# Performance work log

Hardware: AMD Instinct MI355X
Metric: run time of the kernel (lower is better)

## Reference

```python
import math
import jax, jax.numpy as jnp
import numpy as np


def _precompute_psi(nlat_in, nlon_in, nlat_out, K, theta_cutoff):
    """Faithful numpy port of _precompute_convolution_tensor (equiangular grids).
    Returns COO indices (k, t, lat_in, lon_in) and float values of the sparse
    filter tensor psi of logical shape [K, nlat_out, nlat_in*nlon_in]."""
    lats_in = np.linspace(0.0, np.pi, nlat_in)
    lats_out = np.linspace(0.0, np.pi, nlat_out)
    phis = np.linspace(-np.pi, np.pi, nlon_in)
    d_theta = theta_cutoff / K
    theta_i = np.arange(K) * d_theta  # (K,)
    ks, ts, las, los, vs = [], [], [], [], []
    alpha = -lats_in[:, None]          # (nlat_in, 1)
    beta = phis[None, :]               # (1, nlon_in)
    for t in range(nlat_out):
        gamma = lats_out[t]
        z = np.cos(alpha) * np.cos(gamma) - np.cos(beta) * np.sin(alpha) * np.sin(gamma)
        theta = np.arccos(np.clip(z, -1.0, 1.0))   # (nlat_in, nlon_in)
        diff = np.abs(theta[None, :, :] - theta_i[:, None, None])  # (K, nlat_in, nlon_in)
        mask = (diff < d_theta) & (theta[None, :, :] < theta_cutoff)
        k_idx, la_idx, lo_idx = np.nonzero(mask)
        v = 1.0 - diff[k_idx, la_idx, lo_idx] / d_theta  # triangle (hat) weights
        ks.append(k_idx); ts.append(np.full_like(k_idx, t)); las.append(la_idx); los.append(lo_idx); vs.append(v)
    return (np.concatenate(ks).astype(np.int32),
            np.concatenate(ts).astype(np.int32),
            np.concatenate(las).astype(np.int32),
            np.concatenate(los).astype(np.int32),
            np.concatenate(vs).astype(np.float32))


def setup_inputs() -> dict:
    B, C = 4, 32
    nlat_in, nlon_in = 361, 720
    nlat_out, nlon_out = 361, 720
    K = 3
    theta_cutoff = 0.01 * math.pi  # default used at the precompute call site
    k, t, la, lo, v = _precompute_psi(nlat_in, nlon_in, nlat_out, K, theta_cutoff)
    key = jax.random.key(0)
    x = jax.random.normal(key, (B, C, nlat_in, nlon_in), dtype=jnp.float32)
    return {
        "x": x,
        "psi_vals": jnp.asarray(v),
        "psi_k": jnp.asarray(k),
        "psi_t": jnp.asarray(t),
        "psi_lat": jnp.asarray(la),
        "psi_lon": jnp.asarray(lo),
        "kernel_size": K,
        "nlat_out": nlat_out,
        "nlon_out": nlon_out,
    }


def reference(x, psi_vals, psi_k, psi_t, psi_lat, psi_lon, kernel_size, nlat_out, nlon_out):
    B, C, nlat_in, nlon_in = x.shape
    BC = B * C
    scale = nlon_in // nlon_out  # = 1 here
    # (nlat_in, nlon_in, BC) layout, matching x.reshape(B*C,...).permute(1,2,0)
    xr = x.reshape(BC, nlat_in, nlon_in).transpose(1, 2, 0)
    seg = psi_k * nlat_out + psi_t           # row id in the (K*nlat_out) output
    num_seg = kernel_size * nlat_out

    def step(_, p):
        # torch.roll(x, scale, dims=lon) applied (p+1) times before the bmm:
        # rolled[lat, lon] = x[lat, (lon - (p+1)*scale) % nlon]
        lon_idx = (psi_lon - (p + 1) * scale) % nlon_in
        g = xr[psi_lat, lon_idx]             # (nnz, BC) irregular gather
        out_p = jax.ops.segment_sum(psi_vals[:, None] * g, seg, num_segments=num_seg)
        return None, out_p                   # (K*nlat_out, BC)

    _, outs = jax.lax.scan(step, None, jnp.arange(nlon_out))  # (nlon_out, K*nlat_out, BC)
    outs = outs.reshape(nlon_out, kernel_size, nlat_out, BC)
    # permute(3,1,2,0) then split BC -> (B, C)
    return outs.transpose(3, 1, 2, 0).reshape(B, C, kernel_size, nlat_out, nlon_out)
```

## Files before the change

kernel.cpp:

```cpp
#include <hip/hip_runtime.h>
#include <math.h>


#define NLAT 361
#define NLON 720
#define KK 3
#define PTILE 48
#define NPX 15
#define NT 384
#define PD 56
#define SWN 832
#define TOTCAP (720*1024)

typedef __attribute__((ext_vector_type(8))) short bf16x8;
typedef __attribute__((ext_vector_type(4))) float f32x4;
typedef __attribute__((ext_vector_type(4))) unsigned int u32x4;

#define D_PI 3.14159265358979311599796346854418516159057617187500
#define STEP_LAT (D_PI / 360.0)
#define STEP_PHI ((2.0 * D_PI) / 719.0)
#define CUTOFF (0.01 * D_PI)
#define DTH (CUTOFF / 3.0)

__device__ __forceinline__ void gll16(const void* g, void* l) {
    __builtin_amdgcn_global_load_lds(
        (const __attribute__((address_space(1))) void*)g,
        (__attribute__((address_space(3))) void*)l, 16, 0, 0);
}

__device__ inline unsigned int bf16pair_rne(float lo, float hi) {
    unsigned int a = __builtin_bit_cast(unsigned int, lo);
    unsigned int b = __builtin_bit_cast(unsigned int, hi);
    a = a + 0x7fffu + ((a >> 16) & 1u);
    b = b + 0x7fffu + ((b >> 16) & 1u);
    return (a >> 16) | (b & 0xffff0000u);
}

__global__ __launch_bounds__(512) void bounds_kernel(int4* __restrict__ params,
                                                     float2* __restrict__ pAB,
                                                     unsigned long long* __restrict__ actd) {
    __shared__ int part[512];
    int tid = threadIdx.x;
    int rmins[9], Ws[9], bl8s[9];
    float As[9], Bs[9];
    int wsum = 0;
    if (tid < NLAT) {
        int t = tid;
        double g = (t == 360) ? D_PI : (double)t * STEP_LAT;
        double cg = cos(g), sg = sin(g);
        const double coscut = cos(CUTOFF);
#pragma unroll
        for (int d = 0; d < 9; ++d) {
            int la = t + d - 4;
            int rmin = 0, W = 0;
            double A = 0.0, Bc = 0.0;
            if (la >= 0 && la <= 360) {
                double lad = (la == 360) ? D_PI : (double)la * STEP_LAT;
                A = cos(lad) * cg;
                Bc = sin(lad) * sg;
                if (Bc < 1e-14) {
                    if (A > coscut) { rmin = 0; W = 720; }
                } else {
                    double C = (coscut - A) / Bc;
                    if (C <= -1.0) { rmin = 0; W = 720; }
                    else if (C < 1.0) {
                        double bmax = acos(C);
                        int r0 = (int)floor((D_PI - bmax) / STEP_PHI) + 1;
                        int r1 = (int)ceil((D_PI + bmax) / STEP_PHI) - 1;
                        if (r0 < 0) r0 = 0;
                        if (r1 > 719) r1 = 719;
                        rmin = r0; W = r1 - r0 + 1;
                        if (W < 0) W = 0;
                    }
                }
            }
            rmins[d] = rmin; Ws[d] = W;
            As[d] = (float)A; Bs[d] = (float)Bc;
            int b8 = 0;
            if (W > 0) {
                b8 = (W + 111) & ~7;
                if (b8 > SWN) b8 = SWN;
            }
            bl8s[d] = b8;
            wsum += b8;
        }
    }
    part[tid] = wsum;
    __syncthreads();
    for (int dd = 1; dd < 512; dd <<= 1) {
        int v = part[tid];
        int w2 = (tid >= dd) ? part[tid - dd] : 0;
        __syncthreads();
        part[tid] = v + w2;
        __syncthreads();
    }
    int base = part[tid] - wsum;
    if (tid < NLAT) {
        unsigned long long pk = 0;
        int nact = 0;
#pragma unroll
        for (int d = 0; d < 9; ++d) {
            int off = base;
            base += bl8s[d];
            if (Ws[d] > 0 && off + bl8s[d] <= TOTCAP) {
                params[tid * 9 + d] = make_int4(rmins[d], Ws[d], off, bl8s[d]);
                pAB[tid * 9 + d] = make_float2(As[d], Bs[d]);
                pk |= ((unsigned long long)d) << (4 + 4 * nact);
                nact++;
            } else {
                params[tid * 9 + d] = make_int4(0, 0, 0, 0);
            }
        }
        pk |= (unsigned long long)nact;
        actd[tid] = pk;
    }
}

__global__ __launch_bounds__(128) void fill_w_kernel(const int4* __restrict__ params,
                                                     const float2* __restrict__ pAB,
                                                     unsigned int* __restrict__ wtab) {
    int row = blockIdx.x;
    int4 pr = params[row];
    int W = pr.y;
    if (W <= 0) return;
    int rmin = pr.x, off = pr.z, bl8 = pr.w;
    float2 ab = pAB[row];
    float A = ab.x, Bc = ab.y;
    const float invd = (float)(1.0 / DTH);
    for (int idx = threadIdx.x; idx < bl8; idx += 128) {
        int j = idx - PD;
        float f1 = 1.0e9f, f2 = 1.0e9f;
        if (j >= 0 && j < W) {
            int lo = rmin + j;
            float beta = (lo == 719) ? (float)D_PI : (float)((double)lo * STEP_PHI - D_PI);
            float z = fminf(1.f, fmaxf(-1.f, fmaf(Bc, cosf(beta), A)));
            f1 = acosf(z) * invd;
        }
        if (j + 1 >= 0 && j + 1 < W) {
            int lo = rmin + j + 1;
            float beta = (lo == 719) ? (float)D_PI : (float)((double)lo * STEP_PHI - D_PI);
            float z = fminf(1.f, fmaxf(-1.f, fmaf(Bc, cosf(beta), A)));
            f2 = acosf(z) * invd;
        }
        float w0a = fmaxf(0.f, 1.f - f1);
        float w1a = fmaxf(0.f, 1.f - fabsf(f1 - 1.f));
        float w2a = fmaxf(0.f, 1.f - fabsf(f1 - 2.f));
        float w0b = fmaxf(0.f, 1.f - f2);
        float w1b = fmaxf(0.f, 1.f - fabsf(f2 - 1.f));
        float w2b = fmaxf(0.f, 1.f - fabsf(f2 - 2.f));
        size_t e = (size_t)(off + idx) * 3;
        wtab[e + 0] = bf16pair_rne(w0a, w0b);
        wtab[e + 1] = bf16pair_rne(w1a, w1b);
        wtab[e + 2] = bf16pair_rne(w2a, w2b);
    }
}

__global__ void cvt_x_kernel(const float* __restrict__ x, unsigned int* __restrict__ xb,
                             int n8) {
    for (int i = blockIdx.x * 256 + threadIdx.x; i < n8; i += gridDim.x * 256) {
        f32x4 a = *(const f32x4*)(x + (size_t)i * 8);
        f32x4 b = *(const f32x4*)(x + (size_t)i * 8 + 4);
        u32x4 q;
        q.x = bf16pair_rne(a.x, a.y);
        q.y = bf16pair_rne(a.z, a.w);
        q.z = bf16pair_rne(b.x, b.y);
        q.w = bf16pair_rne(b.z, b.w);
        *(u32x4*)(xb + (size_t)i * 4) = q;
    }
}

template <int USEBF16>
__global__ __launch_bounds__(NT, 4) void dconv_mfma_kernel(
    const float* __restrict__ x, const unsigned short* __restrict__ xb,
    const int4* __restrict__ params, const unsigned long long* __restrict__ actd,
    const unsigned int* __restrict__ wtab, float* __restrict__ out) {
    __shared__ __attribute__((aligned(16))) unsigned char sB[2][128 * 128];

    int bid = blockIdx.x;
    int r = bid & 7;
    int rest = bid >> 3;
    int px = rest % NPX;
    int q = rest / NPX;
    int yp = 8 * q + r;
    if (yp > 360) return;
    int t = (yp & 1) ? (360 - (yp >> 1)) : (yp >> 1);
    int p0 = px * PTILE;
    int tid = threadIdx.x;
    int lane = tid & 63;
    int w = tid >> 6;
    int psub = w >> 1;
    int bc0w = (w & 1) * 64;
    int l15 = lane & 15;
    int l4 = lane >> 4;

    f32x4 acc[4][KK];
#pragma unroll
    for (int n = 0; n < 4; ++n)
#pragma unroll
        for (int k = 0; k < KK; ++k) acc[n][k] = (f32x4){0.f, 0.f, 0.f, 0.f};

    unsigned long long pk = actd[t];
    int nact = (int)(pk & 15ull);

    int c = 0, iact = 0;
    int la = 0, W = 0, off = 0, mbase = 0, shift = 0;
    int nK = 0, nC = 1, ks_lo = 0, ks_hi = -1;

    auto LOADP = [&](int dd) {
        la = t + dd - 4;
        int4 pr = params[t * 9 + dd];
        int rmin = pr.x;
        W = pr.y; off = pr.z;
        int ms0 = rmin - 48 - p0;
        shift = (ms0 + 720) & 7;
        nK = (W + 47 + shift + 31) >> 5;
        nC = (nK + 1) >> 1;
        mbase = (((ms0 - shift) % 720) + 720) % 720;
        int s_off = psub * 16 + 9 - shift;
        int kl = (9 - s_off + 31) >> 5;
        ks_lo = kl < 0 ? 0 : kl;
        int kh = (55 + W - s_off) >> 5;
        ks_hi = kh > nK - 1 ? nK - 1 : kh;
    };

    auto ISSUE = [&](int cc, int pbuf) {
#pragma unroll
        for (int pass = 0; pass < 3; ++pass) {
            int slot = pass * NT + tid;
            if (slot < 1024) {
                int bc = slot >> 3;
                int g = slot & 7;
                int gs = g ^ (bc & 7);
                int mg = mbase + cc * 64 + gs * 8;
                mg -= (mg >= 720) ? 720 : 0;
                mg -= (mg >= 720) ? 720 : 0;
                mg -= (mg >= 720) ? 720 : 0;
                if (USEBF16) {
                    gll16(xb + ((size_t)bc * NLAT + la) * NLON + mg,
                          &sB[pbuf][slot * 16]);
                } else {
                    const float* src = x + ((size_t)bc * NLAT + la) * NLON + mg;
                    f32x4 a = *(const f32x4*)(src);
                    f32x4 b = *(const f32x4*)(src + 4);
                    u32x4 qq;
                    qq.x = bf16pair_rne(a.x, a.y);
                    qq.y = bf16pair_rne(a.z, a.w);
                    qq.z = bf16pair_rne(b.x, b.y);
                    qq.w = bf16pair_rne(b.z, b.w);
                    *(u32x4*)(&sB[pbuf][slot * 16]) = qq;
                }
            }
        }
    };

    LOADP((int)((pk >> 4) & 15ull));
    ISSUE(0, 0);
    int pb = 0;

    while (true) {
        int c2 = c * 2;
        bool do0 = (c2 >= ks_lo) && (c2 <= ks_hi);
        bool do1 = (c2 + 1 >= ks_lo) && (c2 + 1 <= ks_hi);
        int soffS = psub * 16 + 9 - shift;
        int offS = off;
        int pbC = pb;
        bool done = false;
        if (c + 1 < nC) {
            c = c + 1;
        } else if (iact + 1 < nact) {
            iact++;
            c = 0;
            LOADP((int)((pk >> (4 + 4 * iact)) & 15ull));
        } else {
            done = true;
        }
        if (USEBF16) asm volatile("s_waitcnt vmcnt(0)" ::: "memory");
        __syncthreads();
        unsigned int A0[KK][4], A1[KK][4];
        if (do0) {
            int s0 = c2 * 32 + l4 * 8 + soffS + l15;
            const unsigned int* bp = wtab + (size_t)(offS + s0) * 3;
#pragma unroll
            for (int e = 0; e < 4; ++e)
#pragma unroll
                for (int k = 0; k < KK; ++k)
                    A0[k][e] = bp[e * 6 + k];
        }
        if (do1) {
            int s1 = (c2 + 1) * 32 + l4 * 8 + soffS + l15;
            const unsigned int* bp = wtab + (size_t)(offS + s1) * 3;
#pragma unroll
            for (int e = 0; e < 4; ++e)
#pragma unroll
                for (int k = 0; k < KK; ++k)
                    A1[k][e] = bp[e * 6 + k];
        }
        if (!done) {
            pb ^= 1;
            ISSUE(c, pb);
        }
        if (do0) {
            bf16x8 af[KK];
#pragma unroll
            for (int k = 0; k < KK; ++k) {
                u32x4 qf;
                qf.x = A0[k][0]; qf.y = A0[k][1]; qf.z = A0[k][2]; qf.w = A0[k][3];
                af[k] = __builtin_bit_cast(bf16x8, qf);
            }
            int colbase = l4 * 16;
#pragma unroll
            for (int n = 0; n < 4; ++n) {
                int brow = bc0w + n * 16 + l15;
                int colb = colbase ^ ((brow & 7) << 4);
                bf16x8 bfv = *(const bf16x8*)(&sB[pbC][brow * 128 + colb]);
                acc[n][0] = __builtin_amdgcn_mfma_f32_16x16x32_bf16(af[0], bfv, acc[n][0], 0, 0, 0);
                acc[n][1] = __builtin_amdgcn_mfma_f32_16x16x32_bf16(af[1], bfv, acc[n][1], 0, 0, 0);
                acc[n][2] = __builtin_amdgcn_mfma_f32_16x16x32_bf16(af[2], bfv, acc[n][2], 0, 0, 0);
            }
        }
        if (do1) {
            bf16x8 af[KK];
#pragma unroll
            for (int k = 0; k < KK; ++k) {
                u32x4 qf;
                qf.x = A1[k][0]; qf.y = A1[k][1]; qf.z = A1[k][2]; qf.w = A1[k][3];
                af[k] = __builtin_bit_cast(bf16x8, qf);
            }
            int colbase = 64 + l4 * 16;
#pragma unroll
            for (int n = 0; n < 4; ++n) {
                int brow = bc0w + n * 16 + l15;
                int colb = colbase ^ ((brow & 7) << 4);
                bf16x8 bfv = *(const bf16x8*)(&sB[pbC][brow * 128 + colb]);
                acc[n][0] = __builtin_amdgcn_mfma_f32_16x16x32_bf16(af[0], bfv, acc[n][0], 0, 0, 0);
                acc[n][1] = __builtin_amdgcn_mfma_f32_16x16x32_bf16(af[1], bfv, acc[n][1], 0, 0, 0);
                acc[n][2] = __builtin_amdgcn_mfma_f32_16x16x32_bf16(af[2], bfv, acc[n][2], 0, 0, 0);
            }
        }
        if (done) break;
    }

    int p = p0 + psub * 16 + l4 * 4;
#pragma unroll
    for (int n = 0; n < 4; ++n) {
        int bc = bc0w + n * 16 + l15;
#pragma unroll
        for (int k = 0; k < KK; ++k) {
            float* o = out + (((size_t)bc * KK + k) * NLAT + t) * NLON + p;
            *(f32x4*)o = acc[n][k];
        }
    }
}

extern "C" void kernel_launch(void* const* d_in, const int* in_sizes, int n_in,
                              void* d_out, int out_size, void* d_ws, size_t ws_size,
                              hipStream_t stream) {
    const float* x = (const float*)d_in[0];
    float* out = (float*)d_out;

    char* ws = (char*)d_ws;
    int4* params = (int4*)(ws + 0);
    float2* pAB = (float2*)(ws + 53248);
    unsigned long long* actd = (unsigned long long*)(ws + 81920);
    unsigned int* wtab = (unsigned int*)(ws + 90112);
    size_t xb_off = (90112 + (size_t)TOTCAP * 12 + 4095) & ~(size_t)4095;
    size_t xb_bytes = (size_t)128 * NLAT * NLON * 2;
    int use_bf16 = (ws_size >= xb_off + xb_bytes) ? 1 : 0;
    unsigned short* xb = (unsigned short*)(ws + xb_off);

    bounds_kernel<<<1, 512, 0, stream>>>(params, pAB, actd);
    fill_w_kernel<<<NLAT * 9, 128, 0, stream>>>(params, pAB, wtab);

    dim3 grid(8 * NPX * 46, 1, 1);
    if (use_bf16) {
        int n8 = 128 * NLAT * NLON / 8;
        cvt_x_kernel<<<2048, 256, 0, stream>>>(x, (unsigned int*)xb, n8);
        dconv_mfma_kernel<1><<<grid, NT, 0, stream>>>(x, xb, params, actd, wtab, out);
    } else {
        dconv_mfma_kernel<0><<<grid, NT, 0, stream>>>(x, xb, params, actd, wtab, out);
    }
}
```

Before: 308.2 us.

## Triple-buffer LDS tiles with partial vmcnt waits and parity-split weight table

Replaces the double-buffered LDS staging with a three-stage ring: two tiles are issued ahead, and waits use explicit partial vmcnt counts plus raw s_barrier instead of waiting for all loads. The weight table moves from interleaved triples to a planar layout split by k and lane parity, so each lane fetches its A fragment with one 16-byte vector load instead of twelve scalar loads. This is meant to hide global-to-LDS latency and reduce load instruction count. The cost is 48KB of LDS per block, which may lower occupancy, and the hand-counted vmcnt values are fragile.

```diff
diff --git a/kernel.cpp b/kernel.cpp
--- a/kernel.cpp
+++ b/kernel.cpp
@@ -9,18 +9,21 @@
 #define NPX 15
 #define NT 384
 #define PD 56
-#define SWN 832
-#define TOTCAP (720*1024)
+#define TOTCAP_Q (320*1024)
+#define BUFSZ (128*128)
 
 typedef __attribute__((ext_vector_type(8))) short bf16x8;
 typedef __attribute__((ext_vector_type(4))) float f32x4;
 typedef __attribute__((ext_vector_type(4))) unsigned int u32x4;
+typedef unsigned int u32x4a __attribute__((ext_vector_type(4), aligned(4)));
 
 #define D_PI 3.14159265358979311599796346854418516159057617187500
 #define STEP_LAT (D_PI / 360.0)
 #define STEP_PHI ((2.0 * D_PI) / 719.0)
 #define CUTOFF (0.01 * D_PI)
 #define DTH (CUTOFF / 3.0)
+
+#define WAITN(n) asm volatile("s_waitcnt vmcnt(" #n ")" ::: "memory")
 
 __device__ __forceinline__ void gll16(const void* g, void* l) {
     __builtin_amdgcn_global_load_lds(
@@ -41,7 +44,7 @@
                                                      unsigned long long* __restrict__ actd) {
     __shared__ int part[512];
     int tid = threadIdx.x;
-    int rmins[9], Ws[9], bl8s[9];
+    int rmins[9], Ws[9], qcaps[9];
     float As[9], Bs[9];
     int wsum = 0;
     if (tid < NLAT) {
@@ -76,13 +79,9 @@
             }
             rmins[d] = rmin; Ws[d] = W;
             As[d] = (float)A; Bs[d] = (float)Bc;
-            int b8 = 0;
-            if (W > 0) {
-                b8 = (W + 111) & ~7;
-                if (b8 > SWN) b8 = SWN;
-            }
-            bl8s[d] = b8;
-            wsum += b8;
+            int qc = (W > 0) ? (((W + 119) & ~15) >> 1) : 0;
+            qcaps[d] = qc;
+            wsum += qc;
         }
     }
     part[tid] = wsum;
@@ -101,9 +100,9 @@
 #pragma unroll
         for (int d = 0; d < 9; ++d) {
             int off = base;
-            base += bl8s[d];
-            if (Ws[d] > 0 && off + bl8s[d] <= TOTCAP) {
-                params[tid * 9 + d] = make_int4(rmins[d], Ws[d], off, bl8s[d]);
+            base += qcaps[d];
+            if (Ws[d] > 0 && off + qcaps[d] <= TOTCAP_Q) {
+                params[tid * 9 + d] = make_int4(rmins[d], Ws[d], off, qcaps[d]);
                 pAB[tid * 9 + d] = make_float2(As[d], Bs[d]);
                 pk |= ((unsigned long long)d) << (4 + 4 * nact);
                 nact++;
@@ -123,21 +122,25 @@
     int4 pr = params[row];
     int W = pr.y;
     if (W <= 0) return;
-    int rmin = pr.x, off = pr.z, bl8 = pr.w;
+    int rmin = pr.x, offq = pr.z, qcap = pr.w;
     float2 ab = pAB[row];
     float A = ab.x, Bc = ab.y;
     const float invd = (float)(1.0 / DTH);
-    for (int idx = threadIdx.x; idx < bl8; idx += 128) {
-        int j = idx - PD;
+    int tot = qcap * 2;
+    for (int idx = threadIdx.x; idx < tot; idx += 128) {
+        int P = idx & 1;
+        int qq = idx >> 1;
+        int j0 = 2 * qq + P - PD;
+        int j1 = j0 + 1;
         float f1 = 1.0e9f, f2 = 1.0e9f;
-        if (j >= 0 && j < W) {
-            int lo = rmin + j;
+        if (j0 >= 0 && j0 < W) {
+            int lo = rmin + j0;
             float beta = (lo == 719) ? (float)D_PI : (float)((double)lo * STEP_PHI - D_PI);
             float z = fminf(1.f, fmaxf(-1.f, fmaf(Bc, cosf(beta), A)));
             f1 = acosf(z) * invd;
         }
-        if (j + 1 >= 0 && j + 1 < W) {
-            int lo = rmin + j + 1;
+        if (j1 >= 0 && j1 < W) {
+            int lo = rmin + j1;
             float beta = (lo == 719) ? (float)D_PI : (float)((double)lo * STEP_PHI - D_PI);
             float z = fminf(1.f, fmaxf(-1.f, fmaf(Bc, cosf(beta), A)));
             f2 = acosf(z) * invd;
@@ -148,10 +151,9 @@
         float w0b = fmaxf(0.f, 1.f - f2);
         float w1b = fmaxf(0.f, 1.f - fabsf(f2 - 1.f));
         float w2b = fmaxf(0.f, 1.f - fabsf(f2 - 2.f));
-        size_t e = (size_t)(off + idx) * 3;
-        wtab[e + 0] = bf16pair_rne(w0a, w0b);
-        wtab[e + 1] = bf16pair_rne(w1a, w1b);
-        wtab[e + 2] = bf16pair_rne(w2a, w2b);
+        wtab[(0 * 2 + P) * TOTCAP_Q + offq + qq] = bf16pair_rne(w0a, w0b);
+        wtab[(1 * 2 + P) * TOTCAP_Q + offq + qq] = bf16pair_rne(w1a, w1b);
+        wtab[(2 * 2 + P) * TOTCAP_Q + offq + qq] = bf16pair_rne(w2a, w2b);
     }
 }
 
@@ -169,19 +171,21 @@
     }
 }
 
+struct Ph { int la, offq, mbase, shift, c2, W, qcap, valid; };
+
 template <int USEBF16>
 __global__ __launch_bounds__(NT, 4) void dconv_mfma_kernel(
     const float* __restrict__ x, const unsigned short* __restrict__ xb,
     const int4* __restrict__ params, const unsigned long long* __restrict__ actd,
     const unsigned int* __restrict__ wtab, float* __restrict__ out) {
-    __shared__ __attribute__((aligned(16))) unsigned char sB[2][128 * 128];
+    __shared__ __attribute__((aligned(16))) unsigned char sB[3 * BUFSZ];
 
     int bid = blockIdx.x;
     int r = bid & 7;
     int rest = bid >> 3;
     int px = rest % NPX;
-    int q = rest / NPX;
-    int yp = 8 * q + r;
+    int qg = rest / NPX;
+    int yp = 8 * qg + r;
     if (yp > 360) return;
     int t = (yp & 1) ? (360 - (yp >> 1)) : (yp >> 1);
     int p0 = px * PTILE;
@@ -202,28 +206,36 @@
     unsigned long long pk = actd[t];
     int nact = (int)(pk & 15ull);
 
-    int c = 0, iact = 0;
-    int la = 0, W = 0, off = 0, mbase = 0, shift = 0;
-    int nK = 0, nC = 1, ks_lo = 0, ks_hi = -1;
+    int iact = 0, c = 0, gdone = 0;
+    int la = 0, W = 0, offq = 0, qcap = 0, mbase = 0, shift = 0, nK = 0, nC = 1;
 
     auto LOADP = [&](int dd) {
         la = t + dd - 4;
         int4 pr = params[t * 9 + dd];
         int rmin = pr.x;
-        W = pr.y; off = pr.z;
+        W = pr.y; offq = pr.z; qcap = pr.w;
         int ms0 = rmin - 48 - p0;
         shift = (ms0 + 720) & 7;
         nK = (W + 47 + shift + 31) >> 5;
         nC = (nK + 1) >> 1;
         mbase = (((ms0 - shift) % 720) + 720) % 720;
-        int s_off = psub * 16 + 9 - shift;
-        int kl = (9 - s_off + 31) >> 5;
-        ks_lo = kl < 0 ? 0 : kl;
-        int kh = (55 + W - s_off) >> 5;
-        ks_hi = kh > nK - 1 ? nK - 1 : kh;
     };
-
-    auto ISSUE = [&](int cc, int pbuf) {
+    auto nextPh = [&](Ph& p) {
+        if (gdone) { p.valid = 0; return; }
+        p.la = la; p.offq = offq; p.mbase = mbase; p.shift = shift;
+        p.W = W; p.qcap = qcap; p.c2 = c * 2; p.valid = 1;
+        if (c + 1 < nC) {
+            c = c + 1;
+        } else if (iact + 1 < nact) {
+            iact++;
+            c = 0;
+            LOADP((int)((pk >> (4 + 4 * iact)) & 15ull));
+        } else {
+            gdone = 1;
+        }
+    };
+    auto ISSUE = [&](const Ph& p, int pbuf) {
+        unsigned char* dst = sB + pbuf * BUFSZ;
 #pragma unroll
         for (int pass = 0; pass < 3; ++pass) {
             int slot = pass * NT + tid;
@@ -231,15 +243,14 @@
                 int bc = slot >> 3;
                 int g = slot & 7;
                 int gs = g ^ (bc & 7);
-                int mg = mbase + cc * 64 + gs * 8;
+                int mg = p.mbase + p.c2 * 32 + gs * 8;
                 mg -= (mg >= 720) ? 720 : 0;
                 mg -= (mg >= 720) ? 720 : 0;
                 mg -= (mg >= 720) ? 720 : 0;
                 if (USEBF16) {
-                    gll16(xb + ((size_t)bc * NLAT + la) * NLON + mg,
-                          &sB[pbuf][slot * 16]);
+                    gll16(xb + ((size_t)bc * NLAT + p.la) * NLON + mg, dst + slot * 16);
                 } else {
-                    const float* src = x + ((size_t)bc * NLAT + la) * NLON + mg;
+                    const float* src = x + ((size_t)bc * NLAT + p.la) * NLON + mg;
                     f32x4 a = *(const f32x4*)(src);
                     f32x4 b = *(const f32x4*)(src + 4);
                     u32x4 qq;
@@ -247,97 +258,91 @@
                     qq.y = bf16pair_rne(a.z, a.w);
                     qq.z = bf16pair_rne(b.x, b.y);
                     qq.w = bf16pair_rne(b.z, b.w);
-                    *(u32x4*)(&sB[pbuf][slot * 16]) = qq;
+                    *(u32x4*)(dst + slot * 16) = qq;
                 }
             }
         }
     };
 
     LOADP((int)((pk >> 4) & 15ull));
-    ISSUE(0, 0);
-    int pb = 0;
-
-    while (true) {
-        int c2 = c * 2;
-        bool do0 = (c2 >= ks_lo) && (c2 <= ks_hi);
-        bool do1 = (c2 + 1 >= ks_lo) && (c2 + 1 <= ks_hi);
-        int soffS = psub * 16 + 9 - shift;
-        int offS = off;
-        int pbC = pb;
-        bool done = false;
-        if (c + 1 < nC) {
-            c = c + 1;
-        } else if (iact + 1 < nact) {
-            iact++;
-            c = 0;
-            LOADP((int)((pk >> (4 + 4 * iact)) & 15ull));
+    Ph ph0, ph1, ph2;
+    nextPh(ph0); nextPh(ph1); nextPh(ph2);
+    if (ph0.valid) ISSUE(ph0, 0);
+    if (ph1.valid) ISSUE(ph1, 1);
+    int bufi = 0;
+
+    while (ph0.valid) {
+        int s_off = psub * 16 + 9 - ph0.shift;
+        int s0 = ph0.c2 * 32 + l4 * 8 + s_off + l15;
+        int s1 = s0 + 32;
+        int qc4 = ph0.qcap - 4;
+        int P0 = s0 & 1, q0 = s0 >> 1;
+        int P1 = s1 & 1, q1 = s1 >> 1;
+        q0 = (q0 > qc4) ? qc4 : q0;
+        q1 = (q1 > qc4) ? qc4 : q1;
+        u32x4a A0[KK], A1[KK];
+#pragma unroll
+        for (int k = 0; k < KK; ++k) {
+            A0[k] = *(const u32x4a*)(wtab + ((size_t)(2 * k + P0)) * TOTCAP_Q + ph0.offq + q0);
+            A1[k] = *(const u32x4a*)(wtab + ((size_t)(2 * k + P1)) * TOTCAP_Q + ph0.offq + q1);
+        }
+        __builtin_amdgcn_sched_barrier(0);
+        int bufn = (bufi >= 1) ? (bufi - 1) : 2;
+        if (ph2.valid) ISSUE(ph2, bufn);
+        if (USEBF16) {
+            if (w < 4) {
+                if (ph2.valid) { WAITN(12); } else if (ph1.valid) { WAITN(9); } else { WAITN(6); }
+            } else {
+                if (ph2.valid) { WAITN(10); } else if (ph1.valid) { WAITN(8); } else { WAITN(6); }
+            }
+            __builtin_amdgcn_s_barrier();
         } else {
-            done = true;
-        }
-        if (USEBF16) asm volatile("s_waitcnt vmcnt(0)" ::: "memory");
-        __syncthreads();
-        unsigned int A0[KK][4], A1[KK][4];
-        if (do0) {
-            int s0 = c2 * 32 + l4 * 8 + soffS + l15;
-            const unsigned int* bp = wtab + (size_t)(offS + s0) * 3;
-#pragma unroll
-            for (int e = 0; e < 4; ++e)
-#pragma unroll
-                for (int k = 0; k < KK; ++k)
-                    A0[k][e] = bp[e * 6 + k];
-        }
-        if (do1) {
-            int s1 = (c2 + 1) * 32 + l4 * 8 + soffS + l15;
-            const unsigned int* bp = wtab + (size_t)(offS + s1) * 3;
-#pragma unroll
-            for (int e = 0; e < 4; ++e)
-#pragma unroll
-                for (int k = 0; k < KK; ++k)
-                    A1[k][e] = bp[e * 6 + k];
-        }
-        if (!done) {
-            pb ^= 1;
-            ISSUE(c, pb);
-        }
-        if (do0) {
-            bf16x8 af[KK];
-#pragma unroll
-            for (int k = 0; k < KK; ++k) {
-                u32x4 qf;
-                qf.x = A0[k][0]; qf.y = A0[k][1]; qf.z = A0[k][2]; qf.w = A0[k][3];
-                af[k] = __builtin_bit_cast(bf16x8, qf);
-            }
-            int colbase = l4 * 16;
-#pragma unroll
-            for (int n = 0; n < 4; ++n) {
-                int brow = bc0w + n * 16 + l15;
-                int colb = colbase ^ ((brow & 7) << 4);
-                bf16x8 bfv = *(const bf16x8*)(&sB[pbC][brow * 128 + colb]);
-                acc[n][0] = __builtin_amdgcn_mfma_f32_16x16x32_bf16(af[0], bfv, acc[n][0], 0, 0, 0);
-                acc[n][1] = __builtin_amdgcn_mfma_f32_16x16x32_bf16(af[1], bfv, acc[n][1], 0, 0, 0);
-                acc[n][2] = __builtin_amdgcn_mfma_f32_16x16x32_bf16(af[2], bfv, acc[n][2], 0, 0, 0);
-            }
-        }
-        if (do1) {
-            bf16x8 af[KK];
-#pragma unroll
-            for (int k = 0; k < KK; ++k) {
-                u32x4 qf;
-                qf.x = A1[k][0]; qf.y = A1[k][1]; qf.z = A1[k][2]; qf.w = A1[k][3];
-                af[k] = __builtin_bit_cast(bf16x8, qf);
-            }
-            int colbase = 64 + l4 * 16;
-#pragma unroll
-            for (int n = 0; n < 4; ++n) {
-                int brow = bc0w + n * 16 + l15;
-                int colb = colbase ^ ((brow & 7) << 4);
-                bf16x8 bfv = *(const bf16x8*)(&sB[pbC][brow * 128 + colb]);
-                acc[n][0] = __builtin_amdgcn_mfma_f32_16x16x32_bf16(af[0], bfv, acc[n][0], 0, 0, 0);
-                acc[n][1] = __builtin_amdgcn_mfma_f32_16x16x32_bf16(af[1], bfv, acc[n][1], 0, 0, 0);
-                acc[n][2] = __builtin_amdgcn_mfma_f32_16x16x32_bf16(af[2], bfv, acc[n][2], 0, 0, 0);
-            }
-        }
-        if (done) break;
+            __syncthreads();
+        }
+        {
+            int nKS = (ph0.W + 47 + ph0.shift + 31) >> 5;
+            int kl = (9 - s_off + 31) >> 5;
+            if (kl < 0) kl = 0;
+            int kh = (55 + ph0.W - s_off) >> 5;
+            if (kh > nKS - 1) kh = nKS - 1;
+            bool do0 = (ph0.c2 >= kl) && (ph0.c2 <= kh);
+            bool do1 = (ph0.c2 + 1 >= kl) && (ph0.c2 + 1 <= kh);
+            const unsigned char* bbuf = sB + bufi * BUFSZ;
+            if (do0) {
+                bf16x8 af[KK];
+#pragma unroll
+                for (int k = 0; k < KK; ++k) af[k] = __builtin_bit_cast(bf16x8, A0[k]);
+                int colbase = l4 * 16;
+#pragma unroll
+                for (int n = 0; n < 4; ++n) {
+                    int brow = bc0w + n * 16 + l15;
+                    int colb = colbase ^ ((brow & 7) << 4);
+                    bf16x8 bfv = *(const bf16x8*)(bbuf + brow * 128 + colb);
+                    acc[n][0] = __builtin_amdgcn_mfma_f32_16x16x32_bf16(af[0], bfv, acc[n][0], 0, 0, 0);
+                    acc[n][1] = __builtin_amdgcn_mfma_f32_16x16x32_bf16(af[1], bfv, acc[n][1], 0, 0, 0);
+                    acc[n][2] = __builtin_amdgcn_mfma_f32_16x16x32_bf16(af[2], bfv, acc[n][2], 0, 0, 0);
+                }
+            }
+            if (do1) {
+                bf16x8 af[KK];
+#pragma unroll
+                for (int k = 0; k < KK; ++k) af[k] = __builtin_bit_cast(bf16x8, A1[k]);
+                int colbase = 64 + l4 * 16;
+#pragma unroll
+                for (int n = 0; n < 4; ++n) {
+                    int brow = bc0w + n * 16 + l15;
+                    int colb = colbase ^ ((brow & 7) << 4);
+                    bf16x8 bfv = *(const bf16x8*)(bbuf + brow * 128 + colb);
+                    acc[n][0] = __builtin_amdgcn_mfma_f32_16x16x32_bf16(af[0], bfv, acc[n][0], 0, 0, 0);
+                    acc[n][1] = __builtin_amdgcn_mfma_f32_16x16x32_bf16(af[1], bfv, acc[n][1], 0, 0, 0);
+                    acc[n][2] = __builtin_amdgcn_mfma_f32_16x16x32_bf16(af[2], bfv, acc[n][2], 0, 0, 0);
+                }
+            }
+        }
+        if (USEBF16) __builtin_amdgcn_s_barrier();
+        else __syncthreads();
+        ph0 = ph1; ph1 = ph2; nextPh(ph2);
+        bufi = (bufi < 2) ? (bufi + 1) : 0;
     }
 
     int p = p0 + psub * 16 + l4 * 4;
@@ -363,7 +368,7 @@
     float2* pAB = (float2*)(ws + 53248);
     unsigned long long* actd = (unsigned long long*)(ws + 81920);
     unsigned int* wtab = (unsigned int*)(ws + 90112);
-    size_t xb_off = (90112 + (size_t)TOTCAP * 12 + 4095) & ~(size_t)4095;
+    size_t xb_off = (90112 + (size_t)6 * TOTCAP_Q * 4 + 4095) & ~(size_t)4095;
     size_t xb_bytes = (size_t)128 * NLAT * NLON * 2;
     int use_bf16 = (ws_size >= xb_off + xb_bytes) ? 1 : 0;
     unsigned short* xb = (unsigned short*)(ws + xb_off);
```

Result: slower. 340.3 us (+10.4%).
